# Optimization experiments

Measured on AMD Instinct MI355X. Metric: run time of the kernel, lower is better.

## Reference

```python
import jax, jax.numpy as jnp
import numpy as np

NF = 64
G_OFF = 4          # offset groups
K = 9              # 3x3 kernel taps


def lrelu(x):
    return jnp.where(x >= 0, x, 0.1 * x)


def conv3(x, w, b):
    # 3x3 conv, stride 1, pad 1, NCHW / OIHW
    y = jax.lax.conv_general_dilated(
        x, w, window_strides=(1, 1), padding=((1, 1), (1, 1)),
        dimension_numbers=('NCHW', 'OIHW', 'NCHW'))
    return y + b[None, :, None, None]


def deform_conv2d(x, offset, w, b, g_off):
    # torchvision-style DCNv1: 3x3, stride 1, pad 1, weight groups = 1
    B, C, H, W = x.shape
    Cg = C // g_off
    O = w.shape[0]
    # offset layout: [B, 2*g*K, H, W] -> [B, g, K, (dy,dx), H, W]
    off = offset.reshape(B, g_off, K, 2, H, W)
    ky = jnp.repeat(jnp.arange(3), 3).astype(x.dtype)  # kernel row per tap
    kx = jnp.tile(jnp.arange(3), 3).astype(x.dtype)    # kernel col per tap
    py = jnp.arange(H, dtype=x.dtype)[None, :, None] - 1.0 + ky[:, None, None]  # [K,H,1]
    px = jnp.arange(W, dtype=x.dtype)[None, None, :] - 1.0 + kx[:, None, None]  # [K,1,W]
    sy = off[:, :, :, 0] + py[None, None]  # [B,g,K,H,W] sampling rows
    sx = off[:, :, :, 1] + px[None, None]  # [B,g,K,H,W] sampling cols
    y0 = jnp.floor(sy)
    x0 = jnp.floor(sx)
    feat = x.reshape(B, g_off, Cg, H * W)
    acc = jnp.zeros((B, g_off, Cg, K * H * W), dtype=x.dtype)
    for dyc, dxc in ((0.0, 0.0), (0.0, 1.0), (1.0, 0.0), (1.0, 1.0)):
        yc = y0 + dyc
        xc = x0 + dxc
        wgt = (1.0 - jnp.abs(sy - yc)) * (1.0 - jnp.abs(sx - xc))
        valid = (yc >= 0) & (yc < H) & (xc >= 0) & (xc < W)
        wgt = jnp.where(valid, wgt, 0.0)
        idx = (jnp.clip(yc, 0, H - 1).astype(jnp.int32) * W
               + jnp.clip(xc, 0, W - 1).astype(jnp.int32))
        gathered = jnp.take_along_axis(feat, idx.reshape(B, g_off, 1, K * H * W), axis=3)
        acc = acc + gathered * wgt.reshape(B, g_off, 1, K * H * W)
    sampled = acc.reshape(B, C, K, H, W)
    out = jnp.einsum('bckhw,ock->bohw', sampled, w.reshape(O, C, K))
    return out + b[None, :, None, None]


def setup_inputs() -> dict:
    key = jax.random.key(0)
    ks = jax.random.split(key, 16)
    B, H, W = 4, 128, 224
    off_ch = 2 * G_OFF * 9  # 72
    s = 0.05
    inp = {
        'nbr_fea_l': jax.random.normal(ks[0], (B, NF, H, W), jnp.float32),
        'ref_fea_l': jax.random.normal(ks[1], (B, NF, H, W), jnp.float32),
        'w_co1': jax.random.normal(ks[2], (NF, 2 * NF, 3, 3), jnp.float32) * s,
        'b_co1': jnp.zeros((NF,), jnp.float32),
        'w_m1': jax.random.normal(ks[3], (NF, NF, 3, 3), jnp.float32) * s,
        'b_m1': jnp.zeros((NF,), jnp.float32),
        'w_m2': jax.random.normal(ks[4], (NF, NF, 3, 3), jnp.float32) * s,
        'b_m2': jnp.zeros((NF,), jnp.float32),
        'w_m3': jax.random.normal(ks[5], (off_ch, NF, 3, 3), jnp.float32) * 0.01,
        'b_m3': jnp.zeros((off_ch,), jnp.float32),
        'w_dcn': jax.random.normal(ks[6], (NF, NF, 3, 3), jnp.float32) * s,
        'b_dcn': jnp.zeros((NF,), jnp.float32),
    }
    return inp


def reference(nbr_fea_l, ref_fea_l, w_co1, b_co1, w_m1, b_m1, w_m2, b_m2,
              w_m3, b_m3, w_dcn, b_dcn):
    feat = lrelu(conv3(jnp.concatenate([nbr_fea_l, ref_fea_l], axis=1), w_co1, b_co1))
    # MotionNet offset head (assumed 3-layer conv stack)
    off = lrelu(conv3(feat, w_m1, b_m1))
    off = lrelu(conv3(off, w_m2, b_m2))
    off = conv3(off, w_m3, b_m3)  # [B, 2*G*9, H, W]
    return lrelu(deform_conv2d(nbr_fea_l, off, w_dcn, b_dcn, G_OFF))
```

## Files before the change

kernel.cpp:

```cpp
#include <hip/hip_runtime.h>

#define HH 128
#define WW 224
#define HW_ (HH * WW)

typedef short short8 __attribute__((ext_vector_type(8)));
typedef float f32x4 __attribute__((ext_vector_type(4)));
typedef float float2v __attribute__((ext_vector_type(2)));

__device__ __forceinline__ float lrelu_f(float v) { return v >= 0.f ? v : 0.1f * v; }

__device__ __forceinline__ unsigned short f2bf(float f) {
  union { float f; unsigned u; } x; x.f = f;
  unsigned r = x.u + 0x7fff + ((x.u >> 16) & 1);
  return (unsigned short)(r >> 16);
}
__device__ __forceinline__ float bf2f(unsigned short u) {
  union { unsigned u; float f; } x; x.u = ((unsigned)u) << 16; return x.f;
}
__device__ __forceinline__ float asf(unsigned u) {
  union { unsigned u; float f; } x; x.u = u; return x.f;
}

__device__ __forceinline__ void wfrag_one(const float* __restrict__ w,
                                          unsigned short* __restrict__ wt,
                                          int i, int O, int C, int NFT) {
  const int CB = C / 32;
  const int j = i & 7;
  const int lane = (i >> 3) & 63;
  const int fid = i >> 9;
  const int nfg = fid % NFT;
  const int kcb = fid / NFT;
  const int cb = kcb % CB;
  const int k = kcb / CB;
  const int o = nfg * 16 + (lane & 15);
  const int c = cb * 32 + (lane >> 4) * 8 + j;
  float v = (o < O) ? w[((size_t)o * C + c) * 9 + k] : 0.f;
  wt[i] = f2bf(v);
}
__device__ __forceinline__ void wdcn_one(const float* __restrict__ w,
                                         unsigned short* __restrict__ wt, int i) {
  const int j = i & 7;
  const int lane = (i >> 3) & 63;
  const int fid = i >> 9;
  const int mf = fid & 3;
  const int s = (fid >> 2) % 5;
  const int g = fid / 20;
  const int l15 = lane & 15, lg = lane >> 4;
  const int o = mf * 16 + l15;
  const int t = 2 * s + (lg >> 1);
  const int c = g * 16 + (lg & 1) * 8 + j;
  float v = (t < 9) ? w[((size_t)o * 64 + c) * 9 + t] : 0.f;
  wt[i] = f2bf(v);
}

__global__ __launch_bounds__(256)
void prep_all(const float* __restrict__ nbr, const float* __restrict__ ref,
              const float* __restrict__ w1, const float* __restrict__ wm1,
              const float* __restrict__ wm2, const float* __restrict__ wm3,
              const float* __restrict__ wdcn,
              unsigned short* __restrict__ xt, unsigned short* __restrict__ xnb,
              unsigned short* __restrict__ wf1, unsigned short* __restrict__ wfm1,
              unsigned short* __restrict__ wfm2, unsigned short* __restrict__ wfm3,
              unsigned short* __restrict__ wdf) {
  __shared__ __align__(16) char ls[64 * 256];
  if (blockIdx.x >= 1792) {
    int i = (blockIdx.x - 1792) * 256 + threadIdx.x;
    if (i < 73728) { wfrag_one(w1, wf1, i, 64, 128, 4); return; }
    i -= 73728;
    if (i < 36864) { wfrag_one(wm1, wfm1, i, 64, 64, 4); return; }
    i -= 36864;
    if (i < 36864) { wfrag_one(wm2, wfm2, i, 64, 64, 4); return; }
    i -= 36864;
    if (i < 46080) { wfrag_one(wm3, wfm3, i, 72, 64, 5); return; }
    i -= 46080;
    if (i < 40960) wdcn_one(wdcn, wdf, i);
    return;
  }
  const int lane = threadIdx.x & 63;
  const int q = threadIdx.x >> 6;
  const int bxp = blockIdx.x % 448;
  const int b = blockIdx.x / 448;
  const int p0 = bxp * 64;
  const int p = p0 + lane;
  const int c0 = q * 32;
  const float* src = (c0 < 64) ? (nbr + ((size_t)b * 64 + c0) * HW_)
                               : (ref + ((size_t)b * 64 + (c0 - 64)) * HW_);
  unsigned short tmp[32];
  #pragma unroll
  for (int i = 0; i < 32; ++i) tmp[i] = f2bf(src[(size_t)i * HW_ + p]);
  #pragma unroll
  for (int j = 0; j < 4; ++j) {
    const int byte = (c0 * 2 + j * 16) ^ ((lane & 7) << 4);
    *(short8*)(ls + lane * 256 + byte) = *(const short8*)(tmp + j * 8);
  }
  __syncthreads();
  const int tid = threadIdx.x;
  unsigned short* dst = xt + ((size_t)b * HW_ + p0) * 128;
  #pragma unroll
  for (int j = 0; j < 4; ++j) {
    const int unit = tid * 4 + j;
    const int px = unit >> 4, ck = unit & 15;
    const short8 v = *(const short8*)(ls + px * 256 + ((ck * 16) ^ ((px & 7) << 4)));
    *(short8*)(dst + (size_t)px * 128 + ck * 8) = v;
  }
  unsigned short* dst2 = xnb + ((size_t)b * HW_ + p0) * 64;
  #pragma unroll
  for (int j = 0; j < 2; ++j) {
    const int unit = tid * 2 + j;
    const int px = unit >> 3, ck = unit & 7;
    const short8 v = *(const short8*)(ls + px * 256 + ((ck * 16) ^ ((px & 7) << 4)));
    *(short8*)(dst2 + (size_t)px * 64 + ck * 8) = v;
  }
}

template<int CINB, int NFT, int CROW, bool LRELU>
__global__ __launch_bounds__(256, 2)
void conv_lds2(const unsigned short* __restrict__ xt, const unsigned short* __restrict__ wfrag,
               const float* __restrict__ bias, unsigned short* __restrict__ out, int coutReal) {
  __shared__ __align__(16) char xs[10 * 34 * 128];
  const int tid = threadIdx.x;
  const int lane = tid & 63, wv = tid >> 6;
  const int l15 = lane & 15, lg = lane >> 4;
  const int b = blockIdx.y;
  const int ty = (blockIdx.x / 7) * 8, tx = (blockIdx.x % 7) * 32;
  const int CIN = CINB * 64;
  const unsigned short* xb = xt + (size_t)b * HW_ * CIN;

  f32x4 acc[4][NFT];
  #pragma unroll
  for (int mf = 0; mf < 4; ++mf)
    #pragma unroll
    for (int nf = 0; nf < NFT; ++nf) acc[mf][nf] = (f32x4){0.f, 0.f, 0.f, 0.f};

  #pragma unroll 1
  for (int cb2 = 0; cb2 < CINB; ++cb2) {
    if (cb2 > 0) __syncthreads();
    for (int ci = tid; ci < 2720; ci += 256) {
      const int ch = ci & 7;
      const int hp = ci >> 3;
      const int hr = hp / 34, hc = hp % 34;
      const int gy = ty + hr - 1, gx = tx + hc - 1;
      short8 v = (short8)0;
      if (((unsigned)gy < HH) & ((unsigned)gx < WW))
        v = *(const short8*)(xb + (size_t)(gy * WW + gx) * CIN + cb2 * 64 + ch * 8);
      *(short8*)(xs + hp * 128 + ((ch * 16) ^ ((hc & 7) << 4))) = v;
    }
    __syncthreads();

    #pragma unroll
    for (int k = 0; k < 9; ++k) {
      const int ky = k / 3, kx = k % 3;
      #pragma unroll
      for (int cb = 0; cb < 2; ++cb) {
        short8 av[4];
        #pragma unroll
        for (int mf = 0; mf < 4; ++mf) {
          const int hr = 2 * wv + (mf >> 1) + ky;
          const int hc = (mf & 1) * 16 + l15 + kx;
          av[mf] = *(const short8*)(xs + (hr * 34 + hc) * 128
                                    + ((cb * 64 + lg * 16) ^ ((hc & 7) << 4)));
        }
        #pragma unroll
        for (int nf = 0; nf < NFT; ++nf) {
          const short8 bv = *(const short8*)(wfrag
              + ((size_t)((k * (CINB * 2) + cb2 * 2 + cb) * NFT + nf)) * 512 + lane * 8);
          #pragma unroll
          for (int mf = 0; mf < 4; ++mf)
            acc[mf][nf] = __builtin_amdgcn_mfma_f32_16x16x32_bf16(av[mf], bv, acc[mf][nf], 0, 0, 0);
        }
      }
    }
  }

  unsigned short* ob = out + (size_t)b * HW_ * CROW;
  #pragma unroll
  for (int nf = 0; nf < NFT; ++nf) {
    const int o = nf * 16 + l15;
    const bool ov = (o < coutReal);
    const float bz = ov ? bias[o] : 0.f;
    #pragma unroll
    for (int mf = 0; mf < 4; ++mf) {
      const int rr = ty + 2 * wv + (mf >> 1);
      #pragma unroll
      for (int r = 0; r < 4; ++r) {
        const int cc = tx + (mf & 1) * 16 + lg * 4 + r;
        float vv = acc[mf][nf][r] + bz;
        if (LRELU) vv = lrelu_f(vv);
        if (ov) ob[(size_t)(rr * WW + cc) * CROW + o] = f2bf(vv);
      }
    }
  }
}

template<int CINB, int NFT, int CROW, bool LRELU>
__global__ __launch_bounds__(256, 2)
void conv_lds(const unsigned short* __restrict__ xt, const unsigned short* __restrict__ wfrag,
              const float* __restrict__ bias, unsigned short* __restrict__ out, int coutReal) {
  __shared__ __align__(16) char xs[6 * 34 * 128];
  const int tid = threadIdx.x;
  const int lane = tid & 63, wv = tid >> 6;
  const int l15 = lane & 15, lg = lane >> 4;
  const int b = blockIdx.y;
  const int ty = (blockIdx.x / 7) * 4, tx = (blockIdx.x % 7) * 32;
  const int CIN = CINB * 64;
  const unsigned short* xb = xt + (size_t)b * HW_ * CIN;

  f32x4 acc[2][NFT];
  #pragma unroll
  for (int mf = 0; mf < 2; ++mf)
    #pragma unroll
    for (int nf = 0; nf < NFT; ++nf) acc[mf][nf] = (f32x4){0.f, 0.f, 0.f, 0.f};

  #pragma unroll 1
  for (int cb2 = 0; cb2 < CINB; ++cb2) {
    if (cb2 > 0) __syncthreads();
    for (int ci = tid; ci < 1632; ci += 256) {
      const int ch = ci & 7;
      const int hp = ci >> 3;
      const int hr = hp / 34, hc = hp % 34;
      const int gy = ty + hr - 1, gx = tx + hc - 1;
      short8 v = (short8)0;
      if (((unsigned)gy < HH) & ((unsigned)gx < WW))
        v = *(const short8*)(xb + (size_t)(gy * WW + gx) * CIN + cb2 * 64 + ch * 8);
      *(short8*)(xs + hp * 128 + ((ch * 16) ^ ((hc & 7) << 4))) = v;
    }
    __syncthreads();

    #pragma unroll
    for (int k = 0; k < 9; ++k) {
      const int ky = k / 3, kx = k % 3;
      #pragma unroll
      for (int cb = 0; cb < 2; ++cb) {
        short8 av[2];
        #pragma unroll
        for (int mf = 0; mf < 2; ++mf) {
          const int hr = wv + ky;
          const int hc = mf * 16 + l15 + kx;
          av[mf] = *(const short8*)(xs + (hr * 34 + hc) * 128
                                    + ((cb * 64 + lg * 16) ^ ((hc & 7) << 4)));
        }
        #pragma unroll
        for (int nf = 0; nf < NFT; ++nf) {
          const short8 bv = *(const short8*)(wfrag
              + ((size_t)((k * (CINB * 2) + cb2 * 2 + cb) * NFT + nf)) * 512 + lane * 8);
          #pragma unroll
          for (int mf = 0; mf < 2; ++mf)
            acc[mf][nf] = __builtin_amdgcn_mfma_f32_16x16x32_bf16(av[mf], bv, acc[mf][nf], 0, 0, 0);
        }
      }
    }
  }

  unsigned short* ob = out + (size_t)b * HW_ * CROW;
  const int rr = ty + wv;
  #pragma unroll
  for (int nf = 0; nf < NFT; ++nf) {
    const int o = nf * 16 + l15;
    const bool ov = (o < coutReal);
    const float bz = ov ? bias[o] : 0.f;
    #pragma unroll
    for (int mf = 0; mf < 2; ++mf) {
      #pragma unroll
      for (int r = 0; r < 4; ++r) {
        const int cc = tx + mf * 16 + lg * 4 + r;
        float vv = acc[mf][nf][r] + bz;
        if (LRELU) vv = lrelu_f(vv);
        if (ov) ob[(size_t)(rr * WW + cc) * CROW + o] = f2bf(vv);
      }
    }
  }
}

__global__ __launch_bounds__(256, 2)
void dcn_v7(const unsigned short* __restrict__ xnb,
            const unsigned short* __restrict__ offt,
            const unsigned short* __restrict__ wdf,
            const float* __restrict__ bias, float* __restrict__ out) {
  __shared__ __align__(16) char xs[12 * 24 * 128];
  const int tid = threadIdx.x;
  const int w = tid >> 6, l = tid & 63;
  const int l15 = l & 15, lg = l >> 4;
  const int b = blockIdx.y;
  const int bx = blockIdx.x;
  const int swz = (bx & 7) * 56 + (bx >> 3);
  const int tx = (swz % 14) * 16;
  const int ty = (swz / 14) * 4;
  const int y = ty + w;
  const int x = tx + l15;
  const int p_img = y * WW + x;
  const unsigned short* xb = xnb + (size_t)b * HW_ * 64;

  for (int ci = tid; ci < 2304; ci += 256) {
    const int ch = ci & 7;
    const int pos = ci >> 3;
    const int r = pos / 24, c = pos % 24;
    const int gy = ty - 4 + r, gx = tx - 4 + c;
    short8 v = (short8)0;
    if (((unsigned)gy < HH) & ((unsigned)gx < WW))
      v = *(const short8*)(xb + (size_t)(gy * WW + gx) * 64 + ch * 8);
    *(short8*)(xs + pos * 128 + ((ch * 16) ^ (((r + c) & 7) << 4))) = v;
  }
  __syncthreads();

  const unsigned* od = (const unsigned*)(offt + ((size_t)b * HW_ + p_img) * 72);
  const int thalf = lg >> 1;
  const int cofs0 = (lg & 1) * 8;

  float pyA[5], pxA[5];
  int liveA[5];
  #pragma unroll
  for (int s = 0; s < 5; ++s) {
    const int t = 2 * s + thalf;
    liveA[s] = (t < 9);
    const int tt = liveA[s] ? t : 0;
    pyA[s] = (float)(y - 1 + tt / 3);
    pxA[s] = (float)(x - 1 + tt % 3);
  }

  f32x4 acc[4];
  #pragma unroll
  for (int mf = 0; mf < 4; ++mf) acc[mf] = (f32x4){0.f, 0.f, 0.f, 0.f};

  #pragma unroll 1
  for (int g = 0; g < 4; ++g) {
    const int cofs = g * 16 + cofs0;
    const int chunkB = cofs * 2;
    #pragma unroll
    for (int s = 0; s < 5; ++s) {
      const int live = liveA[s];
      const int t = 2 * s + thalf;
      const unsigned dpair = od[g * 9 + (live ? t : 0)];
      const float dy = bf2f((unsigned short)(dpair & 0xffff));
      const float dx = bf2f((unsigned short)(dpair >> 16));
      const float sy = dy + pyA[s];
      const float sx = dx + pxA[s];
      const float fy = floorf(sy);
      const float fx = floorf(sx);
      const int y0 = (int)fy;
      const int x0 = (int)fx;
      const float ay = sy - fy;
      const float ax = sx - fx;
      const float by = 1.f - ay, bxx = 1.f - ax;
      float w00 = by * bxx, w01 = by * ax, w10 = ay * bxx, w11 = ay * ax;
      const int ry0 = y0 - ty + 4;
      const int rx0 = x0 - tx + 4;
      const bool inT = (!live) | (((unsigned)ry0 < 11u) & ((unsigned)rx0 < 23u));
      short8 q00, q01, q10, q11;
      if (__all((int)inT)) {
        const int r0 = live ? ry0 : 0;
        const int c0 = live ? rx0 : 0;
        const int b00 = (r0 * 24 + c0) << 7;
        const int sw00 = b00 + (chunkB ^ (((r0 + c0) & 7) << 4));
        const int sw01 = b00 + 128 + (chunkB ^ (((r0 + c0 + 1) & 7) << 4));
        const int b10 = b00 + 24 * 128;
        const int sw10 = b10 + (chunkB ^ (((r0 + c0 + 1) & 7) << 4));
        const int sw11 = b10 + 128 + (chunkB ^ (((r0 + c0 + 2) & 7) << 4));
        q00 = *(const short8*)(xs + sw00);
        q01 = *(const short8*)(xs + sw01);
        q10 = *(const short8*)(xs + sw10);
        q11 = *(const short8*)(xs + sw11);
      } else {
        const bool vy0 = (y0 >= 0) & (y0 < HH);
        const bool vy1 = (y0 + 1 >= 0) & (y0 + 1 < HH);
        const bool vx0 = (x0 >= 0) & (x0 < WW);
        const bool vx1 = (x0 + 1 >= 0) & (x0 + 1 < WW);
        w00 = (vy0 & vx0) ? w00 : 0.f;
        w01 = (vy0 & vx1) ? w01 : 0.f;
        w10 = (vy1 & vx0) ? w10 : 0.f;
        w11 = (vy1 & vx1) ? w11 : 0.f;
        const int cy0 = min(max(y0, 0), HH - 1);
        const int cy1 = min(max(y0 + 1, 0), HH - 1);
        const int cx0 = min(max(x0, 0), WW - 1);
        const int cx1 = min(max(x0 + 1, 0), WW - 1);
        q00 = *(const short8*)(xb + (size_t)(cy0 * WW + cx0) * 64 + cofs);
        q01 = *(const short8*)(xb + (size_t)(cy0 * WW + cx1) * 64 + cofs);
        q10 = *(const short8*)(xb + (size_t)(cy1 * WW + cx0) * 64 + cofs);
        q11 = *(const short8*)(xb + (size_t)(cy1 * WW + cx1) * 64 + cofs);
      }
      short8 pf = (short8)0;
      if (live) {
        const unsigned* u00 = (const unsigned*)&q00;
        const unsigned* u01 = (const unsigned*)&q01;
        const unsigned* u10 = (const unsigned*)&q10;
        const unsigned* u11 = (const unsigned*)&q11;
        unsigned pr[4];
        #pragma unroll
        for (int i = 0; i < 4; ++i) {
          float2v f00, f01, f10, f11;
          f00.x = asf(u00[i] << 16); f00.y = asf(u00[i] & 0xffff0000u);
          f01.x = asf(u01[i] << 16); f01.y = asf(u01[i] & 0xffff0000u);
          f10.x = asf(u10[i] << 16); f10.y = asf(u10[i] & 0xffff0000u);
          f11.x = asf(u11[i] << 16); f11.y = asf(u11[i] & 0xffff0000u);
          const float2v s2 = f00 * w00 + f01 * w01 + f10 * w10 + f11 * w11;
          unsigned pk;
          asm("v_cvt_pk_bf16_f32 %0, %1, %2" : "=v"(pk) : "v"(s2.x), "v"(s2.y));
          pr[i] = pk;
        }
        pf = *(const short8*)pr;
      }
      #pragma unroll
      for (int mf = 0; mf < 4; ++mf) {
        const short8 wf = *(const short8*)(wdf + ((size_t)((g * 5 + s) * 4 + mf)) * 512 + l * 8);
        acc[mf] = __builtin_amdgcn_mfma_f32_16x16x32_bf16(wf, pf, acc[mf], 0, 0, 0);
      }
    }
  }

  float* ob = out + (size_t)b * 64 * HW_;
  #pragma unroll
  for (int mf = 0; mf < 4; ++mf) {
    #pragma unroll
    for (int r = 0; r < 4; ++r) {
      const int o = mf * 16 + lg * 4 + r;
      ob[(size_t)o * HW_ + p_img] = lrelu_f(acc[mf][r] + bias[o]);
    }
  }
}

extern "C" void kernel_launch(void* const* d_in, const int* in_sizes, int n_in,
                              void* d_out, int out_size, void* d_ws, size_t ws_size,
                              hipStream_t stream) {
  const float* nbr   = (const float*)d_in[0];
  const float* ref   = (const float*)d_in[1];
  const float* w_co1 = (const float*)d_in[2];
  const float* b_co1 = (const float*)d_in[3];
  const float* w_m1  = (const float*)d_in[4];
  const float* b_m1  = (const float*)d_in[5];
  const float* w_m2  = (const float*)d_in[6];
  const float* b_m2  = (const float*)d_in[7];
  const float* w_m3  = (const float*)d_in[8];
  const float* b_m3  = (const float*)d_in[9];
  const float* w_dcn = (const float*)d_in[10];
  const float* b_dcn = (const float*)d_in[11];
  float* out = (float*)d_out;

  char* ws = (char*)d_ws;
  unsigned short* xnb   = (unsigned short*)(ws);
  unsigned short* x1t   = (unsigned short*)(ws + 14680064);
  unsigned short* m1t   = (unsigned short*)(ws + 14680064);
  unsigned short* m2t   = (unsigned short*)(ws + 29360128);
  unsigned short* featt = (unsigned short*)(ws + 44040192);
  unsigned short* offt  = (unsigned short*)(ws + 44040192);
  char* wbase = ws + 60555264;
  unsigned short* wf1  = (unsigned short*)(wbase);
  unsigned short* wfm1 = (unsigned short*)(wbase + 147456);
  unsigned short* wfm2 = (unsigned short*)(wbase + 221184);
  unsigned short* wfm3 = (unsigned short*)(wbase + 294912);
  unsigned short* wdf  = (unsigned short*)(wbase + 387072);

  dim3 blk(256);
  prep_all<<<dim3(2708), blk, 0, stream>>>(nbr, ref, w_co1, w_m1, w_m2, w_m3, w_dcn,
                                           x1t, xnb, wf1, wfm1, wfm2, wfm3, wdf);

  conv_lds2<2, 4, 64, true ><<<dim3(112, 4), blk, 0, stream>>>(x1t,   wf1,  b_co1, featt, 64);
  conv_lds2<1, 4, 64, true ><<<dim3(112, 4), blk, 0, stream>>>(featt, wfm1, b_m1,  m1t,   64);
  conv_lds2<1, 4, 64, true ><<<dim3(112, 4), blk, 0, stream>>>(m1t,   wfm2, b_m2,  m2t,   64);
  conv_lds <1, 5, 72, false><<<dim3(224, 4), blk, 0, stream>>>(m2t,   wfm3, b_m3,  offt,  72);
  dcn_v7<<<dim3(448, 4), blk, 0, stream>>>(xnb, offt, wdf, b_dcn, out);
}
```

Before: 167.1 us.

## Fuse prep and four conv stages into one persistent kernel with grid barriers

Replaces the prep kernel and four separate conv launches with one persistent 448-block kernel that separates stages with an atomic-counter grid barrier, removing launch gaps and tail effects between stages. The deformable conv kernel also gets a smaller LDS halo tile (10x20 instead of 12x24), which cuts staging loads but sends more samples to the slow global-memory fallback path. The grid barrier assumes all 448 blocks are co-resident (two per CU), and each stage now runs at a fixed 448-block parallelism.

```diff
diff --git a/kernel.cpp b/kernel.cpp
--- a/kernel.cpp
+++ b/kernel.cpp
@@ -20,6 +20,18 @@
 }
 __device__ __forceinline__ float asf(unsigned u) {
   union { unsigned u; float f; } x; x.u = u; return x.f;
+}
+
+__device__ __forceinline__ void gbar(unsigned* __restrict__ bar, unsigned target) {
+  __syncthreads();
+  if (threadIdx.x == 0) {
+    __threadfence();
+    __hip_atomic_fetch_add(bar, 1u, __ATOMIC_RELEASE, __HIP_MEMORY_SCOPE_AGENT);
+    while (__hip_atomic_load(bar, __ATOMIC_ACQUIRE, __HIP_MEMORY_SCOPE_AGENT) < target)
+      __builtin_amdgcn_s_sleep(4);
+  }
+  __syncthreads();
+  __threadfence();
 }
 
 __device__ __forceinline__ void wfrag_one(const float* __restrict__ w,
@@ -54,76 +66,16 @@
   wt[i] = f2bf(v);
 }
 
-__global__ __launch_bounds__(256)
-void prep_all(const float* __restrict__ nbr, const float* __restrict__ ref,
-              const float* __restrict__ w1, const float* __restrict__ wm1,
-              const float* __restrict__ wm2, const float* __restrict__ wm3,
-              const float* __restrict__ wdcn,
-              unsigned short* __restrict__ xt, unsigned short* __restrict__ xnb,
-              unsigned short* __restrict__ wf1, unsigned short* __restrict__ wfm1,
-              unsigned short* __restrict__ wfm2, unsigned short* __restrict__ wfm3,
-              unsigned short* __restrict__ wdf) {
-  __shared__ __align__(16) char ls[64 * 256];
-  if (blockIdx.x >= 1792) {
-    int i = (blockIdx.x - 1792) * 256 + threadIdx.x;
-    if (i < 73728) { wfrag_one(w1, wf1, i, 64, 128, 4); return; }
-    i -= 73728;
-    if (i < 36864) { wfrag_one(wm1, wfm1, i, 64, 64, 4); return; }
-    i -= 36864;
-    if (i < 36864) { wfrag_one(wm2, wfm2, i, 64, 64, 4); return; }
-    i -= 36864;
-    if (i < 46080) { wfrag_one(wm3, wfm3, i, 72, 64, 5); return; }
-    i -= 46080;
-    if (i < 40960) wdcn_one(wdcn, wdf, i);
-    return;
-  }
-  const int lane = threadIdx.x & 63;
-  const int q = threadIdx.x >> 6;
-  const int bxp = blockIdx.x % 448;
-  const int b = blockIdx.x / 448;
-  const int p0 = bxp * 64;
-  const int p = p0 + lane;
-  const int c0 = q * 32;
-  const float* src = (c0 < 64) ? (nbr + ((size_t)b * 64 + c0) * HW_)
-                               : (ref + ((size_t)b * 64 + (c0 - 64)) * HW_);
-  unsigned short tmp[32];
-  #pragma unroll
-  for (int i = 0; i < 32; ++i) tmp[i] = f2bf(src[(size_t)i * HW_ + p]);
-  #pragma unroll
-  for (int j = 0; j < 4; ++j) {
-    const int byte = (c0 * 2 + j * 16) ^ ((lane & 7) << 4);
-    *(short8*)(ls + lane * 256 + byte) = *(const short8*)(tmp + j * 8);
-  }
-  __syncthreads();
-  const int tid = threadIdx.x;
-  unsigned short* dst = xt + ((size_t)b * HW_ + p0) * 128;
-  #pragma unroll
-  for (int j = 0; j < 4; ++j) {
-    const int unit = tid * 4 + j;
-    const int px = unit >> 4, ck = unit & 15;
-    const short8 v = *(const short8*)(ls + px * 256 + ((ck * 16) ^ ((px & 7) << 4)));
-    *(short8*)(dst + (size_t)px * 128 + ck * 8) = v;
-  }
-  unsigned short* dst2 = xnb + ((size_t)b * HW_ + p0) * 64;
-  #pragma unroll
-  for (int j = 0; j < 2; ++j) {
-    const int unit = tid * 2 + j;
-    const int px = unit >> 3, ck = unit & 7;
-    const short8 v = *(const short8*)(ls + px * 256 + ((ck * 16) ^ ((px & 7) << 4)));
-    *(short8*)(dst2 + (size_t)px * 64 + ck * 8) = v;
-  }
-}
-
 template<int CINB, int NFT, int CROW, bool LRELU>
-__global__ __launch_bounds__(256, 2)
-void conv_lds2(const unsigned short* __restrict__ xt, const unsigned short* __restrict__ wfrag,
-               const float* __restrict__ bias, unsigned short* __restrict__ out, int coutReal) {
-  __shared__ __align__(16) char xs[10 * 34 * 128];
+__device__ __forceinline__
+void conv_tile8(char* __restrict__ xs, const unsigned short* __restrict__ xt,
+                const unsigned short* __restrict__ wfrag, const float* __restrict__ bias,
+                unsigned short* __restrict__ out, int coutReal, int idx) {
   const int tid = threadIdx.x;
   const int lane = tid & 63, wv = tid >> 6;
   const int l15 = lane & 15, lg = lane >> 4;
-  const int b = blockIdx.y;
-  const int ty = (blockIdx.x / 7) * 8, tx = (blockIdx.x % 7) * 32;
+  const int tile = idx % 112, b = idx / 112;
+  const int ty = (tile / 7) * 8, tx = (tile % 7) * 32;
   const int CIN = CINB * 64;
   const unsigned short* xb = xt + (size_t)b * HW_ * CIN;
 
@@ -193,18 +145,18 @@
   }
 }
 
-template<int CINB, int NFT, int CROW, bool LRELU>
-__global__ __launch_bounds__(256, 2)
-void conv_lds(const unsigned short* __restrict__ xt, const unsigned short* __restrict__ wfrag,
-              const float* __restrict__ bias, unsigned short* __restrict__ out, int coutReal) {
-  __shared__ __align__(16) char xs[6 * 34 * 128];
+template<int NFT, int CROW, bool LRELU>
+__device__ __forceinline__
+void conv_tile4(char* __restrict__ xs, const unsigned short* __restrict__ xt,
+                const unsigned short* __restrict__ wfrag, const float* __restrict__ bias,
+                unsigned short* __restrict__ out, int coutReal, int u) {
+  __syncthreads();
   const int tid = threadIdx.x;
   const int lane = tid & 63, wv = tid >> 6;
   const int l15 = lane & 15, lg = lane >> 4;
-  const int b = blockIdx.y;
-  const int ty = (blockIdx.x / 7) * 4, tx = (blockIdx.x % 7) * 32;
-  const int CIN = CINB * 64;
-  const unsigned short* xb = xt + (size_t)b * HW_ * CIN;
+  const int tile = u % 224, b = u / 224;
+  const int ty = (tile / 7) * 4, tx = (tile % 7) * 32;
+  const unsigned short* xb = xt + (size_t)b * HW_ * 64;
 
   f32x4 acc[2][NFT];
   #pragma unroll
@@ -212,42 +164,38 @@
     #pragma unroll
     for (int nf = 0; nf < NFT; ++nf) acc[mf][nf] = (f32x4){0.f, 0.f, 0.f, 0.f};
 
-  #pragma unroll 1
-  for (int cb2 = 0; cb2 < CINB; ++cb2) {
-    if (cb2 > 0) __syncthreads();
-    for (int ci = tid; ci < 1632; ci += 256) {
-      const int ch = ci & 7;
-      const int hp = ci >> 3;
-      const int hr = hp / 34, hc = hp % 34;
-      const int gy = ty + hr - 1, gx = tx + hc - 1;
-      short8 v = (short8)0;
-      if (((unsigned)gy < HH) & ((unsigned)gx < WW))
-        v = *(const short8*)(xb + (size_t)(gy * WW + gx) * CIN + cb2 * 64 + ch * 8);
-      *(short8*)(xs + hp * 128 + ((ch * 16) ^ ((hc & 7) << 4))) = v;
-    }
-    __syncthreads();
-
-    #pragma unroll
-    for (int k = 0; k < 9; ++k) {
-      const int ky = k / 3, kx = k % 3;
-      #pragma unroll
-      for (int cb = 0; cb < 2; ++cb) {
-        short8 av[2];
+  for (int ci = tid; ci < 1632; ci += 256) {
+    const int ch = ci & 7;
+    const int hp = ci >> 3;
+    const int hr = hp / 34, hc = hp % 34;
+    const int gy = ty + hr - 1, gx = tx + hc - 1;
+    short8 v = (short8)0;
+    if (((unsigned)gy < HH) & ((unsigned)gx < WW))
+      v = *(const short8*)(xb + (size_t)(gy * WW + gx) * 64 + ch * 8);
+    *(short8*)(xs + hp * 128 + ((ch * 16) ^ ((hc & 7) << 4))) = v;
+  }
+  __syncthreads();
+
+  #pragma unroll
+  for (int k = 0; k < 9; ++k) {
+    const int ky = k / 3, kx = k % 3;
+    #pragma unroll
+    for (int cb = 0; cb < 2; ++cb) {
+      short8 av[2];
+      #pragma unroll
+      for (int mf = 0; mf < 2; ++mf) {
+        const int hr = wv + ky;
+        const int hc = mf * 16 + l15 + kx;
+        av[mf] = *(const short8*)(xs + (hr * 34 + hc) * 128
+                                  + ((cb * 64 + lg * 16) ^ ((hc & 7) << 4)));
+      }
+      #pragma unroll
+      for (int nf = 0; nf < NFT; ++nf) {
+        const short8 bv = *(const short8*)(wfrag
+            + ((size_t)((k * 2 + cb) * NFT + nf)) * 512 + lane * 8);
         #pragma unroll
-        for (int mf = 0; mf < 2; ++mf) {
-          const int hr = wv + ky;
-          const int hc = mf * 16 + l15 + kx;
-          av[mf] = *(const short8*)(xs + (hr * 34 + hc) * 128
-                                    + ((cb * 64 + lg * 16) ^ ((hc & 7) << 4)));
-        }
-        #pragma unroll
-        for (int nf = 0; nf < NFT; ++nf) {
-          const short8 bv = *(const short8*)(wfrag
-              + ((size_t)((k * (CINB * 2) + cb2 * 2 + cb) * NFT + nf)) * 512 + lane * 8);
-          #pragma unroll
-          for (int mf = 0; mf < 2; ++mf)
-            acc[mf][nf] = __builtin_amdgcn_mfma_f32_16x16x32_bf16(av[mf], bv, acc[mf][nf], 0, 0, 0);
-        }
+        for (int mf = 0; mf < 2; ++mf)
+          acc[mf][nf] = __builtin_amdgcn_mfma_f32_16x16x32_bf16(av[mf], bv, acc[mf][nf], 0, 0, 0);
       }
     }
   }
@@ -273,11 +221,85 @@
 }
 
 __global__ __launch_bounds__(256, 2)
-void dcn_v7(const unsigned short* __restrict__ xnb,
+void fused_convs(const float* __restrict__ nbr, const float* __restrict__ ref,
+                 const float* __restrict__ w1, const float* __restrict__ wm1,
+                 const float* __restrict__ wm2, const float* __restrict__ wm3,
+                 const float* __restrict__ wdcn,
+                 const float* __restrict__ b1, const float* __restrict__ bm1,
+                 const float* __restrict__ bm2, const float* __restrict__ bm3,
+                 unsigned short* __restrict__ x1t, unsigned short* __restrict__ xnb,
+                 unsigned short* __restrict__ featt, unsigned short* __restrict__ m1t,
+                 unsigned short* __restrict__ m2t, unsigned short* __restrict__ offt,
+                 unsigned short* __restrict__ wf1, unsigned short* __restrict__ wfm1,
+                 unsigned short* __restrict__ wfm2, unsigned short* __restrict__ wfm3,
+                 unsigned short* __restrict__ wdf, unsigned* __restrict__ bar) {
+  __shared__ __align__(16) char xs[10 * 34 * 128];
+  const int bx = blockIdx.x;
+  const int tid = threadIdx.x;
+
+  {
+    const int lane = tid & 63;
+    const int q = tid >> 6;
+    const int c0 = q * 32;
+    const int p0 = bx * 64;
+    const int p = p0 + lane;
+    #pragma unroll 1
+    for (int b = 0; b < 4; ++b) {
+      if (b) __syncthreads();
+      const float* src = (c0 < 64) ? (nbr + ((size_t)b * 64 + c0) * HW_)
+                                   : (ref + ((size_t)b * 64 + (c0 - 64)) * HW_);
+      unsigned short tmp[32];
+      #pragma unroll
+      for (int i = 0; i < 32; ++i) tmp[i] = f2bf(src[(size_t)i * HW_ + p]);
+      #pragma unroll
+      for (int j = 0; j < 4; ++j) {
+        const int byte = (c0 * 2 + j * 16) ^ ((lane & 7) << 4);
+        *(short8*)(xs + lane * 256 + byte) = *(const short8*)(tmp + j * 8);
+      }
+      __syncthreads();
+      unsigned short* dst = x1t + ((size_t)b * HW_ + p0) * 128;
+      #pragma unroll
+      for (int j = 0; j < 4; ++j) {
+        const int unit = tid * 4 + j;
+        const int px = unit >> 4, ck = unit & 15;
+        const short8 v = *(const short8*)(xs + px * 256 + ((ck * 16) ^ ((px & 7) << 4)));
+        *(short8*)(dst + (size_t)px * 128 + ck * 8) = v;
+      }
+      unsigned short* dst2 = xnb + ((size_t)b * HW_ + p0) * 64;
+      #pragma unroll
+      for (int j = 0; j < 2; ++j) {
+        const int unit = tid * 2 + j;
+        const int px = unit >> 3, ck = unit & 7;
+        const short8 v = *(const short8*)(xs + px * 256 + ((ck * 16) ^ ((px & 7) << 4)));
+        *(short8*)(dst2 + (size_t)px * 64 + ck * 8) = v;
+      }
+    }
+  }
+  for (int i = bx * 256 + tid; i < 234496; i += 114688) {
+    if (i < 73728)       wfrag_one(w1,  wf1,  i,          64, 128, 4);
+    else if (i < 110592) wfrag_one(wm1, wfm1, i - 73728,  64, 64, 4);
+    else if (i < 147456) wfrag_one(wm2, wfm2, i - 110592, 64, 64, 4);
+    else if (i < 193536) wfrag_one(wm3, wfm3, i - 147456, 72, 64, 5);
+    else                 wdcn_one(wdcn, wdf,  i - 193536);
+  }
+
+  gbar(bar, 448);
+  conv_tile8<2, 4, 64, true >(xs, x1t,   wf1,  b1,  featt, 64, bx);
+  gbar(bar, 896);
+  conv_tile8<1, 4, 64, true >(xs, featt, wfm1, bm1, m1t,   64, bx);
+  gbar(bar, 1344);
+  conv_tile8<1, 4, 64, true >(xs, m1t,   wfm2, bm2, m2t,   64, bx);
+  gbar(bar, 1792);
+  conv_tile4<5, 72, false>(xs, m2t, wfm3, bm3, offt, 72, bx);
+  conv_tile4<5, 72, false>(xs, m2t, wfm3, bm3, offt, 72, 448 + bx);
+}
+
+__global__ __launch_bounds__(256, 2)
+void dcn_v8(const unsigned short* __restrict__ xnb,
             const unsigned short* __restrict__ offt,
             const unsigned short* __restrict__ wdf,
             const float* __restrict__ bias, float* __restrict__ out) {
-  __shared__ __align__(16) char xs[12 * 24 * 128];
+  __shared__ __align__(16) char xs[10 * 20 * 128];
   const int tid = threadIdx.x;
   const int w = tid >> 6, l = tid & 63;
   const int l15 = l & 15, lg = l >> 4;
@@ -291,11 +313,11 @@
   const int p_img = y * WW + x;
   const unsigned short* xb = xnb + (size_t)b * HW_ * 64;
 
-  for (int ci = tid; ci < 2304; ci += 256) {
+  for (int ci = tid; ci < 1600; ci += 256) {
     const int ch = ci & 7;
     const int pos = ci >> 3;
-    const int r = pos / 24, c = pos % 24;
-    const int gy = ty - 4 + r, gx = tx - 4 + c;
+    const int r = pos / 20, c = pos % 20;
+    const int gy = ty - 3 + r, gx = tx - 2 + c;
     short8 v = (short8)0;
     if (((unsigned)gy < HH) & ((unsigned)gx < WW))
       v = *(const short8*)(xb + (size_t)(gy * WW + gx) * 64 + ch * 8);
@@ -343,17 +365,17 @@
       const float ax = sx - fx;
       const float by = 1.f - ay, bxx = 1.f - ax;
       float w00 = by * bxx, w01 = by * ax, w10 = ay * bxx, w11 = ay * ax;
-      const int ry0 = y0 - ty + 4;
-      const int rx0 = x0 - tx + 4;
-      const bool inT = (!live) | (((unsigned)ry0 < 11u) & ((unsigned)rx0 < 23u));
+      const int ry0 = y0 - ty + 3;
+      const int rx0 = x0 - tx + 2;
+      const bool inT = (!live) | (((unsigned)ry0 < 9u) & ((unsigned)rx0 < 19u));
       short8 q00, q01, q10, q11;
       if (__all((int)inT)) {
         const int r0 = live ? ry0 : 0;
         const int c0 = live ? rx0 : 0;
-        const int b00 = (r0 * 24 + c0) << 7;
+        const int b00 = (r0 * 20 + c0) << 7;
         const int sw00 = b00 + (chunkB ^ (((r0 + c0) & 7) << 4));
         const int sw01 = b00 + 128 + (chunkB ^ (((r0 + c0 + 1) & 7) << 4));
-        const int b10 = b00 + 24 * 128;
+        const int b10 = b00 + 2560;
         const int sw10 = b10 + (chunkB ^ (((r0 + c0 + 1) & 7) << 4));
         const int sw11 = b10 + 128 + (chunkB ^ (((r0 + c0 + 2) & 7) << 4));
         q00 = *(const short8*)(xs + sw00);
@@ -448,14 +470,13 @@
   unsigned short* wfm2 = (unsigned short*)(wbase + 221184);
   unsigned short* wfm3 = (unsigned short*)(wbase + 294912);
   unsigned short* wdf  = (unsigned short*)(wbase + 387072);
-
-  dim3 blk(256);
-  prep_all<<<dim3(2708), blk, 0, stream>>>(nbr, ref, w_co1, w_m1, w_m2, w_m3, w_dcn,
-                                           x1t, xnb, wf1, wfm1, wfm2, wfm3, wdf);
-
-  conv_lds2<2, 4, 64, true ><<<dim3(112, 4), blk, 0, stream>>>(x1t,   wf1,  b_co1, featt, 64);
-  conv_lds2<1, 4, 64, true ><<<dim3(112, 4), blk, 0, stream>>>(featt, wfm1, b_m1,  m1t,   64);
-  conv_lds2<1, 4, 64, true ><<<dim3(112, 4), blk, 0, stream>>>(m1t,   wfm2, b_m2,  m2t,   64);
-  conv_lds <1, 5, 72, false><<<dim3(224, 4), blk, 0, stream>>>(m2t,   wfm3, b_m3,  offt,  72);
-  dcn_v7<<<dim3(448, 4), blk, 0, stream>>>(xnb, offt, wdf, b_dcn, out);
-}
+  unsigned* bar = (unsigned*)(ws + 61024256);
+
+  hipMemsetAsync(bar, 0, 64, stream);
+  fused_convs<<<dim3(448), dim3(256), 0, stream>>>(
+      nbr, ref, w_co1, w_m1, w_m2, w_m3, w_dcn,
+      b_co1, b_m1, b_m2, b_m3,
+      x1t, xnb, featt, m1t, m2t, offt,
+      wf1, wfm1, wfm2, wfm3, wdf, bar);
+  dcn_v8<<<dim3(448, 4), dim3(256), 0, stream>>>(xnb, offt, wdf, b_dcn, out);
+}
```

Measured after the change: 570.0 us. 3.41x slower.
